# Performance work log

Measured on AMD Instinct MI355X. Metric: run time of the kernel, lower is better.

The kernel has to match this reference:

```python
import jax, jax.numpy as jnp
import numpy as np

BETA = 0.9
THRESHOLD = 1.0
SG_A = 0.5  # rectangular surrogate half-width
NUM_LAYERS = 4

@jax.custom_vjp
def spike(v):
    # heaviside fire on (mem - threshold)
    return (v > 0).astype(v.dtype)

def _spike_fwd(v):
    return spike(v), v

def _spike_bwd(v, g):
    # rectangular surrogate gradient: pass-through inside |v| <= a
    return (g * (jnp.abs(v) <= SG_A).astype(g.dtype),)

spike.defvjp(_spike_fwd, _spike_bwd)

def _lif(mem_prev, inp):
    # snntorch Leaky: reset from previous mem (detached), subtract mechanism
    reset = jax.lax.stop_gradient((mem_prev > THRESHOLD).astype(inp.dtype))
    mem = BETA * mem_prev + inp - reset * THRESHOLD
    spk = spike(mem - THRESHOLD)
    return spk, mem

def setup_inputs() -> dict:
    key = jax.random.key(0)
    k0, k1, k2 = jax.random.split(key, 3)
    L, N, OBS, H = 512, 256, 128, 512
    x = jax.random.normal(k0, (L, N, OBS), jnp.float32)
    mem0 = jnp.zeros((NUM_LAYERS + 1, N, H), jnp.float32)
    enc_W = jax.random.normal(k1, (H, OBS), jnp.float32) / np.sqrt(OBS).astype(np.float32)
    enc_b = jnp.zeros((H,), jnp.float32)
    fc_W = jax.random.normal(k2, (NUM_LAYERS, H, H), jnp.float32) / np.sqrt(H).astype(np.float32)
    fc_b = jnp.zeros((NUM_LAYERS, H), jnp.float32)
    return {"x": x, "mem0": mem0, "enc_W": enc_W, "enc_b": enc_b, "fc_W": fc_W, "fc_b": fc_b}

def reference(x, mem0, enc_W, enc_b, fc_W, fc_b):
    # x: [L, N, obs]; mem0: [num_layers+1, N, H]
    def step(mem_stack, x_t):
        spk, m0 = _lif(mem_stack[0], x_t @ enc_W.T + enc_b)  # encoder: Linear + LIF
        mems = [m0]
        for i in range(NUM_LAYERS):
            spk, m = _lif(mem_stack[i + 1], spk @ fc_W[i].T + fc_b[i])
            mems.append(m)
        return jnp.stack(mems), spk
    mem_final, outputs = jax.lax.scan(step, mem0, x)
    # outputs: [L, N, H] spikes of last layer per step; mem_final: final state list (stacked)
    return outputs, mem_final
```

## Files before the change

### kernel.cpp

```cpp
#include <hip/hip_runtime.h>

#define H 512
#define NB 256
#define OBS 128
#define LSTEPS 512
#define TB 8
#define NTB (LSTEPS / TB)
#define NPHASE (NTB + 8)
#define NWG 256
#define NTHR 512
#define PLANE (NB * H)
#define MPLANE ((size_t)TB * NB * 8)
typedef unsigned long long u64;

__global__ __launch_bounds__(256) void prep_weights(const float* __restrict__ enc_W,
                                                    const float* __restrict__ fc_W,
                                                    float* __restrict__ enc_Wt,
                                                    float* __restrict__ fc_Wt) {
    int idx = blockIdx.x * 256 + threadIdx.x;
    int stride = gridDim.x * 256;
    for (int i = idx; i < 4 * H * H; i += stride) {
        int l = i >> 18;
        int k = (i >> 9) & 511;
        int h = i & 511;
        fc_Wt[i] = fc_W[l * H * H + h * H + k];
    }
    for (int i = idx; i < OBS * H; i += stride) {
        int k = i >> 9;
        int h = i & 511;
        enc_Wt[i] = enc_W[h * OBS + k];
    }
}

__device__ __forceinline__ u64 spread2(unsigned int v) {
    u64 z = v;
    z = (z | (z << 16)) & 0x0000FFFF0000FFFFull;
    z = (z | (z << 8))  & 0x00FF00FF00FF00FFull;
    z = (z | (z << 4))  & 0x0F0F0F0F0F0F0F0Full;
    z = (z | (z << 2))  & 0x3333333333333333ull;
    z = (z | (z << 1))  & 0x5555555555555555ull;
    return z;
}
__device__ __forceinline__ u64 spread4(unsigned int v) {
    u64 z = v & 0xFFFFull;
    z = (z | (z << 24)) & 0x000000FF000000FFull;
    z = (z | (z << 12)) & 0x000F000F000F000Full;
    z = (z | (z << 6))  & 0x0303030303030303ull;
    z = (z | (z << 3))  & 0x1111111111111111ull;
    return z;
}

__global__ __launch_bounds__(NTHR, 2) void snn_persistent(
    const float* __restrict__ x,
    const float* __restrict__ mem0,
    const float* __restrict__ enc_b,
    const float* __restrict__ fc_b,
    const float* __restrict__ enc_Wt,
    const float* __restrict__ fc_Wt,
    u64* __restrict__ masks,
    int* __restrict__ bar,
    float* __restrict__ out)
{
    __shared__ float Wsh[513][64];
    __shared__ u64  Msh[TB][32][8];

    const int tid = threadIdx.x;
    const int wg  = blockIdx.x;
    const int wave = tid >> 6;
    const int lane = tid & 63;

    const int layer = wg >> 6;
    const int hs = (wg >> 3) & 7;
    const int g  = wg & 7;
    const int h0 = hs << 6;
    const int n0 = g << 5;
    const int ng = lane >> 4;
    const int hq = lane & 15;
    const int hq4 = hq << 2;
    const int nl = (wave << 2) | ng;

    const int ew  = wg >> 5;
    const int eh0 = ew << 6;
    const int en0 = (wg & 31) << 3;
    const int enl = 2 * wave + (lane >> 5);
    const int en  = en0 + enl;
    const int hp  = lane & 31;
    const int eh  = eh0 + 2 * hp;

    int* slots = bar;
    int* done  = bar + 256;
    int* rel   = bar + 288;
    const int grp = wg & 7;
    const int gidx = wg >> 3;

    const float* Wl = fc_Wt + (size_t)layer * H * H;
    #pragma unroll
    for (int i = 0; i < 16; ++i) {
        int id = tid + NTHR * i;
        int row = id >> 4, c4 = id & 15;
        *(float4*)&Wsh[row][c4 * 4] = *(const float4*)(Wl + (size_t)row * H + h0 + c4 * 4);
    }
    if (tid < 64) Wsh[512][tid] = 0.f;

    const float4 bfc = *(const float4*)(fc_b + layer * H + h0 + hq4);
    float4 mem_fc = *(const float4*)(mem0 + (size_t)(layer + 1) * PLANE +
                                     (size_t)(n0 + nl) * H + h0 + hq4);
    float2 be2 = make_float2(0.f, 0.f);
    float2 mem_e = make_float2(0.f, 0.f);
    if (wave < 4) {
        be2   = *(const float2*)(enc_b + eh);
        mem_e = *(const float2*)(mem0 + (size_t)en * H + eh);
    }

    __syncthreads();

    for (int p = 0; p < NPHASE; ++p) {
        const int  tb_fc  = p - 2 - 2 * layer;
        const bool fc_act = (tb_fc >= 0) && (tb_fc < NTB);
        const bool enc_act = (p < NTB);

        if (tid == 0 && p >= 2) {
            while (__hip_atomic_load(rel + grp * 32,
                                     __ATOMIC_RELAXED, __HIP_MEMORY_SCOPE_AGENT) < p - 1)
                __builtin_amdgcn_s_sleep(1);
        }
        __syncthreads();

        if (fc_act) {
            const u64* msrc = masks + ((size_t)layer * 4 + ((p + 2) & 3)) * MPLANE;
            #pragma unroll
            for (int i = 0; i < 4; ++i) {
                int id = tid + NTHR * i;
                int tt = id >> 8, n_l = (id >> 3) & 31, w = id & 7;
                u64 v = __hip_atomic_load(msrc + ((size_t)tt * NB + n0 + n_l) * 8 + w,
                                          __ATOMIC_RELAXED, __HIP_MEMORY_SCOPE_AGENT);
                Msh[tt][n_l][w] = v;
            }
        }
        __syncthreads();

        if (enc_act && wave < 4) {
            float2 ea[TB];
            #pragma unroll
            for (int tt = 0; tt < TB; ++tt) ea[tt] = make_float2(0.f, 0.f);
            const float* xbase = x + (size_t)(TB * p) * NB * OBS + (size_t)en * OBS;
            for (int k2 = 0; k2 < 64; ++k2) {
                float2 w0 = *(const float2*)(enc_Wt + (size_t)(2 * k2) * H + eh);
                float2 w1 = *(const float2*)(enc_Wt + (size_t)(2 * k2 + 1) * H + eh);
                #pragma unroll
                for (int tt = 0; tt < TB; ++tt) {
                    float2 xv = *(const float2*)(xbase + (size_t)tt * NB * OBS + 2 * k2);
                    ea[tt].x += xv.x * w0.x; ea[tt].y += xv.x * w0.y;
                    ea[tt].x += xv.y * w1.x; ea[tt].y += xv.y * w1.y;
                }
            }
            u64* edst = masks + (size_t)(0 * 4 + (p & 3)) * MPLANE;
            #pragma unroll
            for (int tt = 0; tt < TB; ++tt) {
                float m0, m1;
                {
                    float inp = ea[tt].x + be2.x; float mp = mem_e.x;
                    float reset = (mp > 1.0f) ? 1.0f : 0.0f;
                    m0 = 0.9f * mp + inp - reset; mem_e.x = m0;
                }
                {
                    float inp = ea[tt].y + be2.y; float mp = mem_e.y;
                    float reset = (mp > 1.0f) ? 1.0f : 0.0f;
                    m1 = 0.9f * mp + inp - reset; mem_e.y = m1;
                }
                u64 b0 = __ballot(m0 > 1.0f);
                u64 b1 = __ballot(m1 > 1.0f);
                unsigned int s0 = (unsigned int)(b0 >> (lane & 32));
                unsigned int s1 = (unsigned int)(b1 >> (lane & 32));
                u64 word = spread2(s0) | (spread2(s1) << 1);
                if ((lane & 31) == 0)
                    __hip_atomic_store(edst + ((size_t)tt * NB + en) * 8 + ew, word,
                                       __ATOMIC_RELAXED, __HIP_MEMORY_SCOPE_AGENT);
            }
        }

        if (fc_act) {
            float* outp = out + (size_t)(TB * tb_fc) * PLANE;
            u64* mdst = masks + ((size_t)(layer + 1) * 4 + (p & 3)) * MPLANE;
            #pragma unroll 1
            for (int tt = 0; tt < TB; ++tt) {
                float4 acc = make_float4(0.f, 0.f, 0.f, 0.f);
                #pragma unroll 1
                for (int w = 0; w < 8; ++w) {
                    u64 rem = Msh[tt][nl][w];
                    if (!__any((int)(rem != 0ull))) continue;
                    const int kb = w << 6;
                    const int pop = __popcll(rem);
                    if (pop) {
                        const int nit = (pop + 1) >> 1;
                        int b0 = kb + __builtin_ctzll(rem); rem &= rem - 1;
                        int b1 = rem ? kb + __builtin_ctzll(rem) : 512; rem &= rem - 1;
                        float4 w0 = *(const float4*)&Wsh[b0][hq4];
                        float4 w1 = make_float4(0.f, 0.f, 0.f, 0.f);
                        if (b1 < 512) w1 = *(const float4*)&Wsh[b1][hq4];
                        #pragma unroll 1
                        for (int i = 1; i < nit; ++i) {
                            int c0 = kb + __builtin_ctzll(rem); rem &= rem - 1;
                            int c1 = rem ? kb + __builtin_ctzll(rem) : 512; rem &= rem - 1;
                            float4 u0 = *(const float4*)&Wsh[c0][hq4];
                            float4 u1 = make_float4(0.f, 0.f, 0.f, 0.f);
                            if (c1 < 512) u1 = *(const float4*)&Wsh[c1][hq4];
                            acc.x += w0.x; acc.y += w0.y; acc.z += w0.z; acc.w += w0.w;
                            acc.x += w1.x; acc.y += w1.y; acc.z += w1.z; acc.w += w1.w;
                            w0 = u0; w1 = u1;
                        }
                        acc.x += w0.x; acc.y += w0.y; acc.z += w0.z; acc.w += w0.w;
                        acc.x += w1.x; acc.y += w1.y; acc.z += w1.z; acc.w += w1.w;
                    }
                }
                float4 mnew;
                { float inp = acc.x + bfc.x; float mp = mem_fc.x;
                  float reset = (mp > 1.0f) ? 1.0f : 0.0f; mnew.x = 0.9f * mp + inp - reset; }
                { float inp = acc.y + bfc.y; float mp = mem_fc.y;
                  float reset = (mp > 1.0f) ? 1.0f : 0.0f; mnew.y = 0.9f * mp + inp - reset; }
                { float inp = acc.z + bfc.z; float mp = mem_fc.z;
                  float reset = (mp > 1.0f) ? 1.0f : 0.0f; mnew.z = 0.9f * mp + inp - reset; }
                { float inp = acc.w + bfc.w; float mp = mem_fc.w;
                  float reset = (mp > 1.0f) ? 1.0f : 0.0f; mnew.w = 0.9f * mp + inp - reset; }
                mem_fc = mnew;

                if (layer < 3) {
                    u64 B0 = __ballot(mnew.x > 1.0f);
                    u64 B1 = __ballot(mnew.y > 1.0f);
                    u64 B2 = __ballot(mnew.z > 1.0f);
                    u64 B3 = __ballot(mnew.w > 1.0f);
                    const int sh = ng << 4;
                    u64 word = spread4((unsigned int)(B0 >> sh))
                             | (spread4((unsigned int)(B1 >> sh)) << 1)
                             | (spread4((unsigned int)(B2 >> sh)) << 2)
                             | (spread4((unsigned int)(B3 >> sh)) << 3);
                    if (hq == 0)
                        __hip_atomic_store(mdst + ((size_t)tt * NB + n0 + nl) * 8 + hs, word,
                                           __ATOMIC_RELAXED, __HIP_MEMORY_SCOPE_AGENT);
                } else {
                    float4 s4;
                    s4.x = (mnew.x > 1.0f) ? 1.0f : 0.0f;
                    s4.y = (mnew.y > 1.0f) ? 1.0f : 0.0f;
                    s4.z = (mnew.z > 1.0f) ? 1.0f : 0.0f;
                    s4.w = (mnew.w > 1.0f) ? 1.0f : 0.0f;
                    *(float4*)(outp + (size_t)tt * PLANE + (size_t)(n0 + nl) * H + h0 + hq4) = s4;
                }
            }
        }

        asm volatile("s_waitcnt vmcnt(0)" ::: "memory");
        __syncthreads();
        if (tid == 0) {
            __hip_atomic_store(slots + grp * 32 + gidx, p + 1,
                               __ATOMIC_RELAXED, __HIP_MEMORY_SCOPE_AGENT);
            if (gidx == 0 && p >= 1) {
                const int target = p;
                for (;;) {
                    int all = 1;
                    #pragma unroll
                    for (int i = 0; i < 32; ++i) {
                        int v = __hip_atomic_load(slots + grp * 32 + i,
                                                  __ATOMIC_RELAXED, __HIP_MEMORY_SCOPE_AGENT);
                        all &= (v >= target);
                    }
                    if (all) break;
                }
                __hip_atomic_store(done + grp, target,
                                   __ATOMIC_RELAXED, __HIP_MEMORY_SCOPE_AGENT);
                for (;;) {
                    int all = 1;
                    #pragma unroll
                    for (int i = 0; i < 8; ++i) {
                        int v = __hip_atomic_load(done + i,
                                                  __ATOMIC_RELAXED, __HIP_MEMORY_SCOPE_AGENT);
                        all &= (v >= target);
                    }
                    if (all) break;
                }
                __hip_atomic_store(rel + grp * 32, target,
                                   __ATOMIC_RELAXED, __HIP_MEMORY_SCOPE_AGENT);
            }
        }
    }

    float* outm = out + (size_t)LSTEPS * PLANE;
    if (wave < 4)
        *(float2*)(outm + (size_t)en * H + eh) = mem_e;
    *(float4*)(outm + (size_t)(layer + 1) * PLANE + (size_t)(n0 + nl) * H + h0 + hq4) = mem_fc;
}

extern "C" void kernel_launch(void* const* d_in, const int* in_sizes, int n_in,
                              void* d_out, int out_size, void* d_ws, size_t ws_size,
                              hipStream_t stream) {
    const float* x     = (const float*)d_in[0];
    const float* mem0  = (const float*)d_in[1];
    const float* enc_W = (const float*)d_in[2];
    const float* enc_b = (const float*)d_in[3];
    const float* fc_W  = (const float*)d_in[4];
    const float* fc_b  = (const float*)d_in[5];
    float* out = (float*)d_out;

    float* fc_Wt  = (float*)d_ws;
    float* enc_Wt = fc_Wt + 4 * H * H;
    u64*   masks  = (u64*)(enc_Wt + OBS * H);
    int*   bar    = (int*)(masks + 16 * MPLANE);

    hipMemsetAsync(bar, 0, 544 * sizeof(int), stream);
    prep_weights<<<dim3(512), dim3(256), 0, stream>>>(enc_W, fc_W, enc_Wt, fc_Wt);
    snn_persistent<<<dim3(NWG), dim3(NTHR), 0, stream>>>(
        x, mem0, enc_b, fc_b, enc_Wt, fc_Wt, masks, bar, out);
}
```

Measured before the change: 4.247 ms.

## Batch all timesteps per weight row and add dense path for spike-heavy words

Restructures the FC spike-accumulation so the loop over 64-bit mask words is outer and the loop over the 8 timesteps in a block is inner, keeping 8 float4 accumulators live. For the first NDENSE mask words, when the wave's maximum pair-count exceeds a threshold, it switches to a dense path that loads each weight row once and reuses it across all 8 timesteps via multiply-by-bit, cutting shared-memory reads. Sparse words keep the ctz-based gather. This raises register pressure (32 extra accumulators) and may lower occupancy or cause spills, and the dense path does wasted FMAs on zero bits.

```diff
diff --git a/kernel.cpp b/kernel.cpp
--- a/kernel.cpp
+++ b/kernel.cpp
@@ -9,6 +9,7 @@
 #define NPHASE (NTB + 8)
 #define NWG 256
 #define NTHR 512
+#define NDENSE 5
 #define PLANE (NB * H)
 #define MPLANE ((size_t)TB * NB * 8)
 typedef unsigned long long u64;
@@ -180,47 +181,121 @@
         }
 
         if (fc_act) {
+            float4 acc[TB];
+            #pragma unroll
+            for (int tt = 0; tt < TB; ++tt) acc[tt] = make_float4(0.f, 0.f, 0.f, 0.f);
+
+            #pragma unroll 1
+            for (int w = 0; w < 8; ++w) {
+                u64 m0w = Msh[0][nl][w], m1w = Msh[1][nl][w];
+                u64 m2w = Msh[2][nl][w], m3w = Msh[3][nl][w];
+                u64 m4w = Msh[4][nl][w], m5w = Msh[5][nl][w];
+                u64 m6w = Msh[6][nl][w], m7w = Msh[7][nl][w];
+                u64 anyw = m0w | m1w | m2w | m3w | m4w | m5w | m6w | m7w;
+                if (!__any((int)(anyw != 0ull))) continue;
+                const int kb = w << 6;
+
+                int spc = 0;
+                {
+                    int pp;
+                    pp = (__popcll(m0w) + 1) >> 1; spc += pp;
+                    pp = (__popcll(m1w) + 1) >> 1; spc += pp;
+                    pp = (__popcll(m2w) + 1) >> 1; spc += pp;
+                    pp = (__popcll(m3w) + 1) >> 1; spc += pp;
+                    pp = (__popcll(m4w) + 1) >> 1; spc += pp;
+                    pp = (__popcll(m5w) + 1) >> 1; spc += pp;
+                    pp = (__popcll(m6w) + 1) >> 1; spc += pp;
+                    pp = (__popcll(m7w) + 1) >> 1; spc += pp;
+                    spc = max(spc, __shfl_xor(spc, 16, 64));
+                    spc = max(spc, __shfl_xor(spc, 32, 64));
+                }
+
+                if (w < NDENSE && spc > 16) {
+                    #pragma unroll 1
+                    for (int half = 0; half < 2; ++half) {
+                        unsigned int h0m = (unsigned int)(m0w >> (half * 32));
+                        unsigned int h1m = (unsigned int)(m1w >> (half * 32));
+                        unsigned int h2m = (unsigned int)(m2w >> (half * 32));
+                        unsigned int h3m = (unsigned int)(m3w >> (half * 32));
+                        unsigned int h4m = (unsigned int)(m4w >> (half * 32));
+                        unsigned int h5m = (unsigned int)(m5w >> (half * 32));
+                        unsigned int h6m = (unsigned int)(m6w >> (half * 32));
+                        unsigned int h7m = (unsigned int)(m7w >> (half * 32));
+                        unsigned int anyh = h0m | h1m | h2m | h3m | h4m | h5m | h6m | h7m;
+                        if (!__any((int)(anyh != 0u))) continue;
+                        const float* wrow = &Wsh[kb + half * 32][hq4];
+                        #pragma unroll 1
+                        for (int kk = 0; kk < 32; ++kk) {
+                            float4 wv = *(const float4*)(wrow + (size_t)kk * 64);
+                            float s0 = (float)((h0m >> kk) & 1u);
+                            float s1 = (float)((h1m >> kk) & 1u);
+                            float s2 = (float)((h2m >> kk) & 1u);
+                            float s3 = (float)((h3m >> kk) & 1u);
+                            float s4 = (float)((h4m >> kk) & 1u);
+                            float s5 = (float)((h5m >> kk) & 1u);
+                            float s6 = (float)((h6m >> kk) & 1u);
+                            float s7 = (float)((h7m >> kk) & 1u);
+                            acc[0].x += s0 * wv.x; acc[0].y += s0 * wv.y; acc[0].z += s0 * wv.z; acc[0].w += s0 * wv.w;
+                            acc[1].x += s1 * wv.x; acc[1].y += s1 * wv.y; acc[1].z += s1 * wv.z; acc[1].w += s1 * wv.w;
+                            acc[2].x += s2 * wv.x; acc[2].y += s2 * wv.y; acc[2].z += s2 * wv.z; acc[2].w += s2 * wv.w;
+                            acc[3].x += s3 * wv.x; acc[3].y += s3 * wv.y; acc[3].z += s3 * wv.z; acc[3].w += s3 * wv.w;
+                            acc[4].x += s4 * wv.x; acc[4].y += s4 * wv.y; acc[4].z += s4 * wv.z; acc[4].w += s4 * wv.w;
+                            acc[5].x += s5 * wv.x; acc[5].y += s5 * wv.y; acc[5].z += s5 * wv.z; acc[5].w += s5 * wv.w;
+                            acc[6].x += s6 * wv.x; acc[6].y += s6 * wv.y; acc[6].z += s6 * wv.z; acc[6].w += s6 * wv.w;
+                            acc[7].x += s7 * wv.x; acc[7].y += s7 * wv.y; acc[7].z += s7 * wv.z; acc[7].w += s7 * wv.w;
+                        }
+                    }
+                } else {
+                    #define SPARSE_TT(MT, TTI)                                               \
+                    {                                                                        \
+                        u64 rem = (MT);                                                      \
+                        if (__any((int)(rem != 0ull))) {                                     \
+                            const int pop = __popcll(rem);                                   \
+                            if (pop) {                                                       \
+                                const int nit = (pop + 1) >> 1;                              \
+                                int b0 = kb + __builtin_ctzll(rem); rem &= rem - 1;          \
+                                int b1 = rem ? kb + __builtin_ctzll(rem) : 512; rem &= rem - 1; \
+                                float4 w0 = *(const float4*)&Wsh[b0][hq4];                   \
+                                float4 w1 = make_float4(0.f, 0.f, 0.f, 0.f);                 \
+                                if (b1 < 512) w1 = *(const float4*)&Wsh[b1][hq4];            \
+                                _Pragma("unroll 1")                                          \
+                                for (int i = 1; i < nit; ++i) {                              \
+                                    int c0 = kb + __builtin_ctzll(rem); rem &= rem - 1;      \
+                                    int c1 = rem ? kb + __builtin_ctzll(rem) : 512; rem &= rem - 1; \
+                                    float4 u0 = *(const float4*)&Wsh[c0][hq4];               \
+                                    float4 u1 = make_float4(0.f, 0.f, 0.f, 0.f);             \
+                                    if (c1 < 512) u1 = *(const float4*)&Wsh[c1][hq4];        \
+                                    acc[TTI].x += w0.x; acc[TTI].y += w0.y;                  \
+                                    acc[TTI].z += w0.z; acc[TTI].w += w0.w;                  \
+                                    acc[TTI].x += w1.x; acc[TTI].y += w1.y;                  \
+                                    acc[TTI].z += w1.z; acc[TTI].w += w1.w;                  \
+                                    w0 = u0; w1 = u1;                                        \
+                                }                                                            \
+                                acc[TTI].x += w0.x; acc[TTI].y += w0.y;                      \
+                                acc[TTI].z += w0.z; acc[TTI].w += w0.w;                      \
+                                acc[TTI].x += w1.x; acc[TTI].y += w1.y;                      \
+                                acc[TTI].z += w1.z; acc[TTI].w += w1.w;                      \
+                            }                                                                \
+                        }                                                                    \
+                    }
+                    SPARSE_TT(m0w, 0) SPARSE_TT(m1w, 1) SPARSE_TT(m2w, 2) SPARSE_TT(m3w, 3)
+                    SPARSE_TT(m4w, 4) SPARSE_TT(m5w, 5) SPARSE_TT(m6w, 6) SPARSE_TT(m7w, 7)
+                    #undef SPARSE_TT
+                }
+            }
+
             float* outp = out + (size_t)(TB * tb_fc) * PLANE;
             u64* mdst = masks + ((size_t)(layer + 1) * 4 + (p & 3)) * MPLANE;
-            #pragma unroll 1
+            #pragma unroll
             for (int tt = 0; tt < TB; ++tt) {
-                float4 acc = make_float4(0.f, 0.f, 0.f, 0.f);
-                #pragma unroll 1
-                for (int w = 0; w < 8; ++w) {
-                    u64 rem = Msh[tt][nl][w];
-                    if (!__any((int)(rem != 0ull))) continue;
-                    const int kb = w << 6;
-                    const int pop = __popcll(rem);
-                    if (pop) {
-                        const int nit = (pop + 1) >> 1;
-                        int b0 = kb + __builtin_ctzll(rem); rem &= rem - 1;
-                        int b1 = rem ? kb + __builtin_ctzll(rem) : 512; rem &= rem - 1;
-                        float4 w0 = *(const float4*)&Wsh[b0][hq4];
-                        float4 w1 = make_float4(0.f, 0.f, 0.f, 0.f);
-                        if (b1 < 512) w1 = *(const float4*)&Wsh[b1][hq4];
-                        #pragma unroll 1
-                        for (int i = 1; i < nit; ++i) {
-                            int c0 = kb + __builtin_ctzll(rem); rem &= rem - 1;
-                            int c1 = rem ? kb + __builtin_ctzll(rem) : 512; rem &= rem - 1;
-                            float4 u0 = *(const float4*)&Wsh[c0][hq4];
-                            float4 u1 = make_float4(0.f, 0.f, 0.f, 0.f);
-                            if (c1 < 512) u1 = *(const float4*)&Wsh[c1][hq4];
-                            acc.x += w0.x; acc.y += w0.y; acc.z += w0.z; acc.w += w0.w;
-                            acc.x += w1.x; acc.y += w1.y; acc.z += w1.z; acc.w += w1.w;
-                            w0 = u0; w1 = u1;
-                        }
-                        acc.x += w0.x; acc.y += w0.y; acc.z += w0.z; acc.w += w0.w;
-                        acc.x += w1.x; acc.y += w1.y; acc.z += w1.z; acc.w += w1.w;
-                    }
-                }
                 float4 mnew;
-                { float inp = acc.x + bfc.x; float mp = mem_fc.x;
+                { float inp = acc[tt].x + bfc.x; float mp = mem_fc.x;
                   float reset = (mp > 1.0f) ? 1.0f : 0.0f; mnew.x = 0.9f * mp + inp - reset; }
-                { float inp = acc.y + bfc.y; float mp = mem_fc.y;
+                { float inp = acc[tt].y + bfc.y; float mp = mem_fc.y;
                   float reset = (mp > 1.0f) ? 1.0f : 0.0f; mnew.y = 0.9f * mp + inp - reset; }
-                { float inp = acc.z + bfc.z; float mp = mem_fc.z;
+                { float inp = acc[tt].z + bfc.z; float mp = mem_fc.z;
                   float reset = (mp > 1.0f) ? 1.0f : 0.0f; mnew.z = 0.9f * mp + inp - reset; }
-                { float inp = acc.w + bfc.w; float mp = mem_fc.w;
+                { float inp = acc[tt].w + bfc.w; float mp = mem_fc.w;
                   float reset = (mp > 1.0f) ? 1.0f : 0.0f; mnew.w = 0.9f * mp + inp - reset; }
                 mem_fc = mnew;
 
```

New measurement: 4.931 ms. 1.16x slower.
